# Optimization experiments

Measured on AMD Instinct MI355X. Metric: run time of the kernel, lower is better.

The kernel has to match this reference:

```python
import jax, jax.numpy as jnp
import numpy as np

B, S, H, NH, EHH, L = 8, 4, 50, 200, 400, 2
HID = 128
FDIM = 44 + 20 + 15          # 79: atom one-hot + amino-acid one-hot + position one-hot
EDIM = 2 * FDIM + 3          # h_i, h_j, distance, bond, t -> 161


def setup_inputs() -> dict:
    key = jax.random.key(0)
    ks = jax.random.split(key, 32)
    inp = {}
    inp["t"] = jax.random.uniform(ks[0], (B,), dtype=jnp.float32)
    inp["x_h"] = jax.random.normal(ks[1], (B, S, H, 3), dtype=jnp.float32)
    inp["x_heavy"] = jax.random.normal(ks[2], (B, 1, NH, 3), dtype=jnp.float32)
    inp["bond_matrix_h_heavy"] = (jax.random.uniform(ks[3], (B, H, NH)) < 0.02).astype(jnp.float32)
    inp["edge_mask_h_heavy"] = jnp.ones((B, H, NH), jnp.float32)
    inp["edge_mask_h_h"] = jnp.ones((B, EHH), jnp.float32)
    inp["atom_mask"] = jnp.ones((B, H, 1), jnp.float32)
    sc = 0.02
    shapes = {"W1": (L, EDIM, HID), "b1": (L, HID), "W2": (L, HID, HID), "b2": (L, HID),
              "Wc1": (L, HID, HID), "bc1": (L, HID), "Wc2": (L, HID, 1),
              "Wn1": (L, FDIM + HID, HID), "bn1": (L, HID), "Wn2": (L, HID, FDIM), "bn2": (L, FDIM)}
    for i, (n, s) in enumerate(shapes.items()):
        inp[n] = jax.random.normal(ks[4 + i], s, dtype=jnp.float32) * sc
    inp["peptide_seq"] = jax.random.randint(ks[20], (B, 15), 0, 20)
    inp["atom_labels_heavy"] = jax.random.randint(ks[21], (B, NH), 0, 44)
    inp["atom_labels_h"] = jax.random.randint(ks[22], (B, H), 0, 44)
    inp["amino_acid_pos_heavy"] = jax.random.randint(ks[23], (B, NH), 1, 16)
    inp["amino_acid_pos_h"] = jax.random.randint(ks[24], (B, H), 1, 16)
    inp["edges_h_h"] = jax.random.randint(ks[25], (B, EHH, 2), 0, H)
    inp["bound_atom"] = jax.random.randint(ks[26], (B, H), 0, NH)
    return inp


def _embed(labels, pos, peptide_seq):
    # one_hot(atom,44) ++ one_hot(seq[pos-1],20) ++ one_hot(pos-1,15)
    aa = jnp.take_along_axis(peptide_seq, pos - 1, axis=1)
    return jnp.concatenate([jax.nn.one_hot(labels, 44, dtype=jnp.float32),
                            jax.nn.one_hot(aa, 20, dtype=jnp.float32),
                            jax.nn.one_hot(pos - 1, 15, dtype=jnp.float32)], axis=-1)


def _gather_nodes(feat, idx):
    # feat [B,S,N,D], idx [B,E] -> [B,S,E,D]
    return jnp.take_along_axis(feat, idx[:, None, :, None], axis=2)


def _seg(data, ids, n):
    # data [B,S,E,D], ids [B,E] -> scatter-add over edges -> [B,S,n,D]
    f = jax.vmap(lambda d, i: jax.ops.segment_sum(jnp.swapaxes(d, 0, 1), i, num_segments=n))
    return jnp.swapaxes(f(data, ids), 1, 2)


def _forward(t, x_h, x_heavy, bond_hm, em_hheavy, em_hh, atom_mask,
             W1, b1, W2, b2, Wc1, bc1, Wc2, Wn1, bn1, Wn2, bn2,
             peptide_seq, atom_labels_heavy, atom_labels_h, pos_heavy, pos_h,
             edges_h_h, bound_atom):
    Bq, Sq, Hq, _ = x_h.shape
    Nh = x_heavy.shape[2]
    xhv = jnp.broadcast_to(x_heavy, (Bq, Sq, Nh, 3))
    emb_h = _embed(atom_labels_h, pos_h, peptide_seq)          # [B,H,79]
    emb_hv = _embed(atom_labels_heavy, pos_heavy, peptide_seq)  # [B,NH,79]
    # absolute coords: x_h relative to its bound heavy atom
    x_h_abs = x_h + jnp.take_along_axis(xhv, bound_atom[:, None, :, None], axis=2)
    x = jnp.concatenate([x_h_abs, xhv], axis=2)                 # [B,S,N,3]
    feat = jnp.concatenate([emb_h, emb_hv], axis=1)             # [B,N,79]
    feat = jnp.broadcast_to(feat[:, None], (Bq, Sq) + feat.shape[1:])
    bond = jnp.concatenate([jnp.zeros((Bq, Hq, Hq), bond_hm.dtype), bond_hm], axis=-1)  # [B,H,N]
    # edge indices: sparse h-h edges, then full h x heavy grid (row-major, cols offset by H)
    grid_r = jnp.repeat(jnp.arange(Hq), Nh)
    grid_c = Hq + jnp.tile(jnp.arange(Nh), Hq)
    edge_row = jnp.concatenate([edges_h_h[..., 0], jnp.broadcast_to(grid_r, (Bq, Hq * Nh))], axis=-1)
    edge_col = jnp.concatenate([edges_h_h[..., 1], jnp.broadcast_to(grid_c, (Bq, Hq * Nh))], axis=-1)
    emask = jnp.concatenate([em_hh, em_hheavy.reshape(Bq, -1)], axis=-1)[:, None, :, None]  # [B,1,E,1]
    bond_e = jax.vmap(lambda bm, r, c: bm[r, c])(bond, edge_row, edge_col)[:, None, :, None]
    x0 = x
    for l in range(W1.shape[0]):
        xi = _gather_nodes(x, edge_row)
        xj = _gather_nodes(x, edge_col)
        diff = xi - xj                                          # [B,S,E,3]
        dist = jnp.linalg.norm(diff, axis=-1, keepdims=True)    # [B,S,E,1]
        hi = _gather_nodes(feat, edge_row)
        hj = _gather_nodes(feat, edge_col)
        t_e = jnp.broadcast_to(t[:, None, None, None], dist.shape)
        ef = jnp.concatenate([hi, hj, dist, jnp.broadcast_to(bond_e, dist.shape), t_e], axis=-1)
        m = jax.nn.silu(ef @ W1[l] + b1[l])
        m = jax.nn.silu(m @ W2[l] + b2[l]) * emask              # masked messages [B,S,E,HID]
        cw = jax.nn.silu(m @ Wc1[l] + bc1[l]) @ Wc2[l]          # [B,S,E,1]
        agg_x = _seg(diff * cw, edge_row, Hq)                   # [B,S,H,3]
        agg_m = _seg(m, edge_row, Hq)                           # [B,S,H,HID]
        h_h = feat[:, :, :Hq]
        h_out = h_h + jax.nn.silu(jnp.concatenate([h_h, agg_m], axis=-1) @ Wn1[l] + bn1[l]) @ Wn2[l] + bn2[l]
        x = jnp.concatenate([x[:, :, :Hq] + agg_x, x[:, :, Hq:]], axis=2)
        feat = jnp.concatenate([h_out, feat[:, :, Hq:]], axis=2)
    pred = (x[:, :, :Hq] - x0[:, :, :Hq]) * atom_mask[:, None, :, :]
    return pred


def reference(t, x_h, x_heavy, bond_matrix_h_heavy, edge_mask_h_heavy, edge_mask_h_h, atom_mask,
              W1, b1, W2, b2, Wc1, bc1, Wc2, Wn1, bn1, Wn2, bn2,
              peptide_seq, atom_labels_heavy, atom_labels_h, amino_acid_pos_heavy, amino_acid_pos_h,
              edges_h_h, bound_atom):
    return _forward(t, x_h, x_heavy, bond_matrix_h_heavy, edge_mask_h_heavy, edge_mask_h_h, atom_mask,
                    W1, b1, W2, b2, Wc1, bc1, Wc2, Wn1, bn1, Wn2, bn2,
                    peptide_seq, atom_labels_heavy, atom_labels_h, amino_acid_pos_heavy, amino_acid_pos_h,
                    edges_h_h, bound_atom)
```

## Files before the change

### kernel.cpp

```cpp
#include <hip/hip_runtime.h>
#include <math.h>

#define B_     8
#define S_     4
#define H_     50
#define NH_    200
#define EHH_   400
#define L_     2
#define HID_   128
#define FDIM_  79
#define EDIM_  161
#define NN_    250
#define NROW_  1600
#define BS_    32
#define FS_    80
#define MSTR_  136
#define NDIM_  207
#define HVB_   1600

#define OFF_FEATH  0
#define OFF_X0     128000
#define OFF_X1     160000
#define OFF_X0H    192000
#define OFF_HHCOL  198400
#define OFF_HHEM   201600
#define OFF_HHOFF  204800
#define OFF_HIW1   205312
#define OFF_HJW1   614912
#define OFF_WP     1434112

typedef __attribute__((ext_vector_type(8))) short short8;
typedef __attribute__((ext_vector_type(4))) float f32x4;

__device__ __forceinline__ float silu_(float v) {
    return v * __builtin_amdgcn_rcpf(1.0f + __expf(-v));
}
__device__ __forceinline__ unsigned short f2bf(float f) {
    unsigned int u = __float_as_uint(f);
    unsigned int r = (u + 0x7fffu + ((u >> 16) & 1u)) >> 16;
    return (unsigned short)r;
}

#define HV_BLKS_    1600
#define PACK_BLKS_  256
#define SORT_BLKS_  8
#define HROW_BLKS_  200
#define FEAT_BLKS_  125
#define XI_BLKS_    32
#define SETUP_BLKS_ (HV_BLKS_ + PACK_BLKS_ + SORT_BLKS_ + HROW_BLKS_ + FEAT_BLKS_ + XI_BLKS_)

__global__ __launch_bounds__(256) void k_setup(
    const float* __restrict__ x_h, const float* __restrict__ x_hv,
    const int* __restrict__ bound,
    const int* __restrict__ ehh, const float* __restrict__ em_hh,
    const float* __restrict__ W1, const float* __restrict__ b1,
    const float* __restrict__ t_in,
    const float* __restrict__ W2, const float* __restrict__ Wc1,
    const int* __restrict__ lab_h, const int* __restrict__ pos_h,
    const int* __restrict__ lab_hv, const int* __restrict__ pos_hv,
    const int* __restrict__ pep,
    float* __restrict__ feat_h,
    float* __restrict__ x0, float* __restrict__ x1, float* __restrict__ x0h,
    int* __restrict__ hhcol, float* __restrict__ hhem, int* __restrict__ hhoff,
    float* __restrict__ hiW1, float* __restrict__ hjW1,
    unsigned short* __restrict__ Wp)
{
    int blk = blockIdx.x, t = threadIdx.x;
    if (blk < HV_BLKS_) {
        int g = blk*256 + t;
        int l = g / 204800;
        int r = g - l*204800;
        int node = r >> 7, col = r & 127;
        int b = node / NH_;
        int label = lab_hv[node], pos = pos_hv[node];
        int aa = pep[b*15 + pos - 1];
        const float* W1l = W1 + l*EDIM_*HID_;
        float hj = W1l[(FDIM_ + label)*HID_ + col]
                 + W1l[(FDIM_ + 44 + aa)*HID_ + col]
                 + W1l[(FDIM_ + 64 + pos - 1)*HID_ + col];
        hjW1[(size_t)(HVB_ + l*1600 + node)*HID_ + col] = hj;
        return;
    }
    blk -= HV_BLKS_;
    if (blk < PACK_BLKS_) {
        int g = blk*256 + t;
        int idx = g & 16383;
        int lm  = g >> 14;
        int l = lm >> 1, mat = lm & 1;
        int j   = idx & 7;
        int l15 = (idx >> 3) & 15;
        int qq  = (idx >> 7) & 3;
        int nt  = (idx >> 9) & 7;
        int kc  = (idx >> 12) & 3;
        int n = nt*16 + l15;
        int k = kc*32 + qq*8 + j;
        const float* W = (mat == 0 ? W2 : Wc1) + l*HID_*HID_;
        Wp[g] = f2bf(W[k*HID_ + n]);
        return;
    }
    blk -= PACK_BLKS_;
    if (blk < SORT_BLKS_) {
        int b = blk;
        __shared__ int scnt[64];
        __shared__ int srow[EHH_], scol[EHH_];
        __shared__ float sem[EHH_];
        if (t < 64) scnt[t] = 0;
        __syncthreads();
        for (int e = t; e < EHH_; e += 256) {
            int r = ehh[(b*EHH_ + e)*2 + 0];
            srow[e] = r;
            scol[e] = ehh[(b*EHH_ + e)*2 + 1];
            sem[e]  = em_hh[b*EHH_ + e];
            atomicAdd(&scnt[r], 1);
        }
        __syncthreads();
        if (t == 0) {
            int acc = 0;
            for (int i = 0; i < H_; ++i) { int v = scnt[i]; scnt[i] = acc; acc += v; }
        }
        __syncthreads();
        if (t < 51) hhoff[b*64 + t] = (t < H_) ? scnt[t] : EHH_;
        __syncthreads();
        for (int e = t; e < EHH_; e += 256) {
            int r = srow[e];
            int pos = atomicAdd(&scnt[r], 1);
            hhcol[b*EHH_ + pos] = scol[e];
            hhem [b*EHH_ + pos] = sem[e];
        }
        return;
    }
    blk -= SORT_BLKS_;
    if (blk < HROW_BLKS_) {
        int g = blk*256 + t;
        int node = g >> 7, col = g & 127;
        int b = node / H_;
        int label = lab_h[node], pos = pos_h[node];
        int aa = pep[b*15 + pos - 1];
        const float* W1l = W1;
        float hi = W1l[label*HID_ + col]
                 + W1l[(44 + aa)*HID_ + col]
                 + W1l[(64 + pos - 1)*HID_ + col]
                 + b1[col]
                 + t_in[b] * W1l[160*HID_ + col];
        float hj = W1l[(FDIM_ + label)*HID_ + col]
                 + W1l[(FDIM_ + 44 + aa)*HID_ + col]
                 + W1l[(FDIM_ + 64 + pos - 1)*HID_ + col];
        int h = node % H_;
        #pragma unroll
        for (int s = 0; s < S_; ++s) {
            int row = (b*S_ + s)*H_ + h;
            hiW1[(size_t)row*HID_ + col] = hi;
            hjW1[(size_t)row*HID_ + col] = hj;
        }
        return;
    }
    blk -= HROW_BLKS_;
    if (blk < FEAT_BLKS_) {
        int g = blk*256 + t;
        int node = g / FS_, f = g % FS_;
        int b = node / H_, h = node % H_;
        int label = lab_h[node], pos = pos_h[node];
        int aa = pep[b*15 + pos - 1];
        float v = 0.f;
        if (f < 44)      v = (f == label)          ? 1.0f : 0.0f;
        else if (f < 64) v = ((f - 44) == aa)      ? 1.0f : 0.0f;
        else if (f < 79) v = ((f - 64) == pos - 1) ? 1.0f : 0.0f;
        #pragma unroll
        for (int s = 0; s < S_; ++s)
            feat_h[((b*S_ + s)*H_ + h)*FS_ + f] = v;
        return;
    }
    blk -= FEAT_BLKS_;
    {
        int g = blk*256 + t;
        if (g >= BS_*NN_) return;
        int bs = g / NN_, n = g % NN_;
        int b = bs / S_;
        if (n < H_) {
            int ba = bound[b*H_ + n];
            for (int d = 0; d < 3; ++d) {
                float v = x_h[(bs*H_ + n)*3 + d] + x_hv[(b*NH_ + ba)*3 + d];
                x0[g*4 + d] = v;
                x0h[(bs*H_ + n)*4 + d] = v;
            }
        } else {
            int nh = n - H_;
            for (int d = 0; d < 3; ++d) {
                float v = x_hv[(b*NH_ + nh)*3 + d];
                x0[g*4 + d] = v;
                x1[g*4 + d] = v;
            }
        }
    }
}

__global__ __launch_bounds__(512) void k_edge_mlp(
    const float* __restrict__ xin, const float* __restrict__ hiW1g,
    const float* __restrict__ hjW1,
    const int* __restrict__ hhcol, const float* __restrict__ hhem,
    const int* __restrict__ hhoff,
    const float* __restrict__ em_hv, const float* __restrict__ bond_in,
    const float* __restrict__ W1,
    const float* __restrict__ b2, const float* __restrict__ bc1,
    const float* __restrict__ Wc2,
    const unsigned short* __restrict__ Wp, int l,
    const float* __restrict__ Wn1, const float* __restrict__ bn1,
    const float* __restrict__ Wn2, const float* __restrict__ bn2,
    const float* __restrict__ b1, const float* __restrict__ t_in,
    float* __restrict__ feat_h, float* __restrict__ xout,
    float* __restrict__ hiW1w, float* __restrict__ hjW1w,
    const float* __restrict__ x0h, const float* __restrict__ amask,
    float* __restrict__ out, int do_w1)
{
    __shared__ unsigned short s_wp[2*16384];
    __shared__ unsigned short s_m[8][16][MSTR_];
    __shared__ float s_hi[8][HID_];
    __shared__ float s_cc[5][HID_];
    __shared__ float s_mr[8][HID_];
    __shared__ float s_xr[8][4];

    const int t = threadIdx.x, lane = t & 63, w = t >> 6;
    const int l15 = lane & 15, q = lane >> 4;
    const int node0 = blockIdx.x*8;
    const int node  = node0 + w;
    const int bs = node / H_, h = node - bs*H_;
    const int b  = bs / S_;
    const int hb = (l ? 4800 : 0) + bs*H_;

    {
        const float4* src = (const float4*)(Wp + (size_t)l*32768);
        float4* dst = (float4*)s_wp;
        #pragma unroll
        for (int i = 0; i < 8; ++i) dst[t + i*512] = src[t + i*512];
    }
    const float* W1l = W1 + l*EDIM_*HID_;
    #pragma unroll
    for (int i = 0; i < 2; ++i) {
        int idx = i*512 + t;
        int g = idx >> 7, c = idx & 127;
        s_hi[g][c] = hiW1g[(size_t)(l*1600 + node0 + g)*HID_ + c];
    }
    if (t < 128) {
        s_cc[0][t] = W1l[158*HID_ + t];
        s_cc[1][t] = W1l[159*HID_ + t];
        s_cc[2][t] = b2 [l*HID_ + t];
        s_cc[3][t] = bc1[l*HID_ + t];
        s_cc[4][t] = Wc2[l*HID_ + t];
    }

    const int hh0 = hhoff[b*64 + h];
    const int cnt = hhoff[b*64 + h + 1] - hh0;
    const int E   = cnt + NH_;
    const int NT  = (E + 15) >> 4;

    const float xi0 = xin[(bs*NN_ + h)*4 + 0];
    const float xi1 = xin[(bs*NN_ + h)*4 + 1];
    const float xi2 = xin[(bs*NN_ + h)*4 + 2];

    auto gather = [&](int e, float& d0, float& d1, float& d2,
                      float& dist, float& bnd, float& em, int& jj) {
        if (e < E) {
            int col;
            if (e < cnt) {
                col = hhcol[b*EHH_ + hh0 + e];
                em  = hhem [b*EHH_ + hh0 + e];
                jj  = hb + col;
            } else {
                int cc = e - cnt;
                col = H_ + cc;
                em  = em_hv [(b*H_ + h)*NH_ + cc];
                bnd = bond_in[(b*H_ + h)*NH_ + cc];
                jj  = HVB_ + l*1600 + b*NH_ + cc;
            }
            d0 = xi0 - xin[(bs*NN_ + col)*4 + 0];
            d1 = xi1 - xin[(bs*NN_ + col)*4 + 1];
            d2 = xi2 - xin[(bs*NN_ + col)*4 + 2];
            dist = sqrtf(d0*d0 + d1*d1 + d2*d2);
        }
    };

    float macc[8] = {0.f,0.f,0.f,0.f,0.f,0.f,0.f,0.f};
    float xacc = 0.f;
    __syncthreads();

    float cd0=0.f, cd1=0.f, cd2=0.f, cdist=0.f, cbnd=0.f, cem=0.f;
    int   cjj = hb;
    if (lane < 16) gather(lane, cd0, cd1, cd2, cdist, cbnd, cem, cjj);
    float distb = __shfl(cdist, l15, 64);
    float bndb  = __shfl(cbnd,  l15, 64);
    int   jjb   = __shfl(cjj,   l15, 64);
    float4 pr[8];
    {
        const float* pj = hjW1 + (size_t)jjb*HID_ + q*8;
        #pragma unroll
        for (int kc = 0; kc < 4; ++kc) {
            pr[2*kc]   = *(const float4*)(pj + kc*32);
            pr[2*kc+1] = *(const float4*)(pj + kc*32 + 4);
        }
    }

    for (int ti = 0; ti < NT; ++ti) {
        const int nx = ti + 1;
        const bool hasNext = (nx < NT);

        float nd0=0.f, nd1=0.f, nd2=0.f, ndist=0.f, nbnd=0.f, nem=0.f;
        int   njj = hb;
        if (hasNext && lane < 16)
            gather(nx*16 + lane, nd0, nd1, nd2, ndist, nbnd, nem, njj);

        short8 afrag[4];
        #pragma unroll
        for (int kc = 0; kc < 4; ++kc) {
            int k0 = kc*32 + q*8;
            float4 c0 = pr[2*kc];
            float4 c1 = pr[2*kc+1];
            float4 h0 = *(const float4*)&s_hi[w][k0];
            float4 h1 = *(const float4*)&s_hi[w][k0 + 4];
            float4 wa0= *(const float4*)&s_cc[0][k0];
            float4 wa1= *(const float4*)&s_cc[0][k0 + 4];
            float4 wb0= *(const float4*)&s_cc[1][k0];
            float4 wb1= *(const float4*)&s_cc[1][k0 + 4];
            short8 fr;
            fr[0] = (short)f2bf(silu_(h0.x + c0.x + distb*wa0.x + bndb*wb0.x));
            fr[1] = (short)f2bf(silu_(h0.y + c0.y + distb*wa0.y + bndb*wb0.y));
            fr[2] = (short)f2bf(silu_(h0.z + c0.z + distb*wa0.z + bndb*wb0.z));
            fr[3] = (short)f2bf(silu_(h0.w + c0.w + distb*wa0.w + bndb*wb0.w));
            fr[4] = (short)f2bf(silu_(h1.x + c1.x + distb*wa1.x + bndb*wb1.x));
            fr[5] = (short)f2bf(silu_(h1.y + c1.y + distb*wa1.y + bndb*wb1.y));
            fr[6] = (short)f2bf(silu_(h1.z + c1.z + distb*wa1.z + bndb*wb1.z));
            fr[7] = (short)f2bf(silu_(h1.w + c1.w + distb*wa1.w + bndb*wb1.w));
            afrag[kc] = fr;
        }

        float ndistb = 0.f, nbndb = 0.f;
        if (hasNext) {
            ndistb = __shfl(ndist, l15, 64);
            nbndb  = __shfl(nbnd,  l15, 64);
            int njjb = __shfl(njj, l15, 64);
            const float* pj = hjW1 + (size_t)njjb*HID_ + q*8;
            #pragma unroll
            for (int kc = 0; kc < 4; ++kc) {
                pr[2*kc]   = *(const float4*)(pj + kc*32);
                pr[2*kc+1] = *(const float4*)(pj + kc*32 + 4);
            }
        }

        float em4[4];
        #pragma unroll
        for (int rr = 0; rr < 4; ++rr) em4[rr] = __shfl(cem, q*4 + rr, 64);
        #pragma unroll
        for (int nt = 0; nt < 8; ++nt) {
            float bias = s_cc[2][nt*16 + l15];
            f32x4 c = {bias, bias, bias, bias};
            #pragma unroll
            for (int kc = 0; kc < 4; ++kc) {
                short8 bf = *(const short8*)&s_wp[((kc*8 + nt)*64 + lane)*8];
                c = __builtin_amdgcn_mfma_f32_16x16x32_bf16(afrag[kc], bf, c, 0, 0, 0);
            }
            #pragma unroll
            for (int rr = 0; rr < 4; ++rr) {
                float mv = silu_(c[rr]) * em4[rr];
                s_m[w][q*4 + rr][nt*16 + l15] = f2bf(mv);
                macc[nt] += mv;
            }
        }
        __builtin_amdgcn_wave_barrier();

        short8 af2[4];
        #pragma unroll
        for (int kc = 0; kc < 4; ++kc)
            af2[kc] = *(const short8*)&s_m[w][l15][kc*32 + q*8];
        float p[4] = {0.f, 0.f, 0.f, 0.f};
        #pragma unroll
        for (int nt = 0; nt < 8; ++nt) {
            float bias = s_cc[3][nt*16 + l15];
            f32x4 c = {bias, bias, bias, bias};
            #pragma unroll
            for (int kc = 0; kc < 4; ++kc) {
                short8 bf = *(const short8*)&s_wp[16384 + ((kc*8 + nt)*64 + lane)*8];
                c = __builtin_amdgcn_mfma_f32_16x16x32_bf16(af2[kc], bf, c, 0, 0, 0);
            }
            float wcv = s_cc[4][nt*16 + l15];
            #pragma unroll
            for (int rr = 0; rr < 4; ++rr)
                p[rr] += silu_(c[rr]) * wcv;
        }
        #pragma unroll
        for (int m = 1; m < 16; m <<= 1) {
            #pragma unroll
            for (int rr = 0; rr < 4; ++rr) p[rr] += __shfl_xor(p[rr], m, 64);
        }
        #pragma unroll
        for (int rr = 0; rr < 4; ++rr) {
            float sd0 = __shfl(cd0, q*4 + rr, 64);
            float sd1 = __shfl(cd1, q*4 + rr, 64);
            float sd2 = __shfl(cd2, q*4 + rr, 64);
            if (l15 < 3) {
                float dsel = (l15 == 0) ? sd0 : ((l15 == 1) ? sd1 : sd2);
                xacc += dsel * p[rr];
            }
        }
        __builtin_amdgcn_wave_barrier();

        cd0 = nd0; cd1 = nd1; cd2 = nd2; cem = nem;
        distb = ndistb; bndb = nbndb;
    }

    #pragma unroll
    for (int nt = 0; nt < 8; ++nt) {
        macc[nt] += __shfl_xor(macc[nt], 16, 64);
        macc[nt] += __shfl_xor(macc[nt], 32, 64);
    }
    if (q == 0) {
        #pragma unroll
        for (int nt = 0; nt < 8; ++nt) s_mr[w][nt*16 + l15] = macc[nt];
    }
    xacc += __shfl_xor(xacc, 16, 64);
    xacc += __shfl_xor(xacc, 32, 64);
    if (q == 0 && l15 < 3) s_xr[w][l15] = xacc;
    __syncthreads();

    float* su = (float*)s_wp;
    for (int idx = t; idx < 8*208; idx += 512) {
        int g = idx / 208, k = idx - g*208;
        float v;
        if (k < FDIM_) v = feat_h[(node0 + g)*FS_ + k];
        else           v = s_mr[g][k - FDIM_];
        su[g*208 + k] = v;
    }
    __syncthreads();
    {
        const float* Wn1l = Wn1 + l*NDIM_*HID_;
        #pragma unroll
        for (int pass = 0; pass < 2; ++pass) {
            int task = pass*512 + t;
            int g = task >> 7, c = task & 127;
            const float* sp = su + g*208;
            const float* wp = Wn1l + c;
            float acc = 0.f;
            #pragma unroll 8
            for (int k = 0; k < NDIM_; ++k)
                acc += sp[k] * wp[(size_t)k*HID_];
            su[2048 + task] = silu_(acc + bn1[l*HID_ + c]);
        }
    }
    __syncthreads();
    {
        const float* Wn2l = Wn2 + l*HID_*FDIM_;
        #pragma unroll
        for (int pass = 0; pass < 2; ++pass) {
            int task = pass*512 + t;
            int g = task >> 7, c = task & 127;
            if (c < FDIM_) {
                const float* up = su + 2048 + g*HID_;
                const float* wp = Wn2l + c;
                float acc = bn2[l*FDIM_ + c];
                #pragma unroll 8
                for (int k = 0; k < HID_; ++k)
                    acc += up[k] * wp[(size_t)k*FDIM_];
                float nf = su[g*208 + c] + acc;
                feat_h[(node0 + g)*FS_ + c] = nf;
                su[g*208 + c] = nf;
            }
        }
    }
    if (t < 24) {
        int g = t / 3, d = t - (t/3)*3;
        int ng = node0 + g;
        int bsg = ng / H_, hg = ng - bsg*H_;
        float xv = xin[(bsg*NN_ + hg)*4 + d] + s_xr[g][d];
        if (do_w1) {
            xout[(bsg*NN_ + hg)*4 + d] = xv;
        } else {
            int bg = bsg / S_;
            out[ng*3 + d] = (xv - x0h[ng*4 + d]) * amask[bg*H_ + hg];
        }
    }
    if (!do_w1) return;
    __syncthreads();
    {
        const float* W1n = W1 + EDIM_*HID_;
        #pragma unroll
        for (int pass = 0; pass < 4; ++pass) {
            int task = pass*512 + t;
            int c = task & 127, g = (task >> 7) & 7, sel = task >> 10;
            const float* sp = su + g*208;
            const float* wp = W1n + (size_t)(sel ? FDIM_ : 0)*HID_ + c;
            float acc = 0.f;
            #pragma unroll 8
            for (int f = 0; f < FDIM_; ++f)
                acc += sp[f] * wp[(size_t)f*HID_];
            int ng = node0 + g;
            if (sel == 0) {
                int bg = (ng / H_) / S_;
                hiW1w[(size_t)(1600 + ng)*HID_ + c] =
                    acc + b1[HID_ + c] + t_in[bg]*W1n[160*HID_ + c];
            } else {
                hjW1w[(size_t)(4800 + ng)*HID_ + c] = acc;
            }
        }
    }
}

extern "C" void kernel_launch(void* const* d_in, const int* in_sizes, int n_in,
                              void* d_out, int out_size, void* d_ws, size_t ws_size,
                              hipStream_t stream)
{
    const float* t_in  = (const float*)d_in[0];
    const float* x_h   = (const float*)d_in[1];
    const float* x_hv  = (const float*)d_in[2];
    const float* bond  = (const float*)d_in[3];
    const float* em_hv = (const float*)d_in[4];
    const float* em_hh = (const float*)d_in[5];
    const float* amask = (const float*)d_in[6];
    const float* W1    = (const float*)d_in[7];
    const float* b1    = (const float*)d_in[8];
    const float* W2    = (const float*)d_in[9];
    const float* b2    = (const float*)d_in[10];
    const float* Wc1   = (const float*)d_in[11];
    const float* bc1   = (const float*)d_in[12];
    const float* Wc2   = (const float*)d_in[13];
    const float* Wn1   = (const float*)d_in[14];
    const float* bn1   = (const float*)d_in[15];
    const float* Wn2   = (const float*)d_in[16];
    const float* bn2   = (const float*)d_in[17];
    const int* pep     = (const int*)d_in[18];
    const int* lab_hv  = (const int*)d_in[19];
    const int* lab_h   = (const int*)d_in[20];
    const int* pos_hv  = (const int*)d_in[21];
    const int* pos_h   = (const int*)d_in[22];
    const int* ehh     = (const int*)d_in[23];
    const int* bound   = (const int*)d_in[24];

    float* ws     = (float*)d_ws;
    float* feat_h = ws + OFF_FEATH;
    float* x0     = ws + OFF_X0;
    float* x1     = ws + OFF_X1;
    float* x0h    = ws + OFF_X0H;
    int*   hhcol  = (int*)(ws + OFF_HHCOL);
    float* hhem   = ws + OFF_HHEM;
    int*   hhoff  = (int*)(ws + OFF_HHOFF);
    float* hiW1   = ws + OFF_HIW1;
    float* hjW1   = ws + OFF_HJW1;
    unsigned short* Wp = (unsigned short*)(ws + OFF_WP);

    hipLaunchKernelGGL(k_setup, dim3(SETUP_BLKS_), dim3(256), 0, stream,
                       x_h, x_hv, bound, ehh, em_hh,
                       W1, b1, t_in, W2, Wc1,
                       lab_h, pos_h, lab_hv, pos_hv, pep,
                       feat_h, x0, x1, x0h, hhcol, hhem, hhoff,
                       hiW1, hjW1, Wp);

    hipLaunchKernelGGL(k_edge_mlp, dim3(NROW_/8), dim3(512), 0, stream,
                       x0, hiW1, hjW1, hhcol, hhem, hhoff, em_hv, bond,
                       W1, b2, bc1, Wc2, Wp, 0,
                       Wn1, bn1, Wn2, bn2, b1, t_in,
                       feat_h, x1, hiW1, hjW1, x0h, amask,
                       (float*)d_out, 1);

    hipLaunchKernelGGL(k_edge_mlp, dim3(NROW_/8), dim3(512), 0, stream,
                       x1, hiW1, hjW1, hhcol, hhem, hhoff, em_hv, bond,
                       W1, b2, bc1, Wc2, Wp, 1,
                       Wn1, bn1, Wn2, bn2, b1, t_in,
                       feat_h, x1, hiW1, hjW1, x0h, amask,
                       (float*)d_out, 0);
}
```

Baseline: 322.7 us.

## Process two edge tiles per loop iteration to interleave independent MFMA chains

The per-node edge loop now handles two 16-edge tiles per iteration (A and B). It gathers and prefetches both tiles' data together and runs their two MFMA accumulator chains interleaved, so each B-fragment loaded from shared memory is reused by both. The intent is to hide MFMA dependency latency and halve the per-tile loop overhead and weight-fragment LDS reads. In exchange it doubles the s_m scratch in shared memory and raises register pressure. It also relies on an odd tile count being safe, with the extra tile gathering padded or masked edges.

```diff
diff --git a/kernel.cpp b/kernel.cpp
--- a/kernel.cpp
+++ b/kernel.cpp
@@ -213,7 +213,7 @@
     float* __restrict__ out, int do_w1)
 {
     __shared__ unsigned short s_wp[2*16384];
-    __shared__ unsigned short s_m[8][16][MSTR_];
+    __shared__ unsigned short s_m[8][2][16][MSTR_];
     __shared__ float s_hi[8][HID_];
     __shared__ float s_cc[5][HID_];
     __shared__ float s_mr[8][HID_];
@@ -283,127 +283,177 @@
     float xacc = 0.f;
     __syncthreads();
 
-    float cd0=0.f, cd1=0.f, cd2=0.f, cdist=0.f, cbnd=0.f, cem=0.f;
-    int   cjj = hb;
-    if (lane < 16) gather(lane, cd0, cd1, cd2, cdist, cbnd, cem, cjj);
-    float distb = __shfl(cdist, l15, 64);
-    float bndb  = __shfl(cbnd,  l15, 64);
-    int   jjb   = __shfl(cjj,   l15, 64);
-    float4 pr[8];
+    float cd0A=0.f, cd1A=0.f, cd2A=0.f, cdistA=0.f, cbndA=0.f, cemA=0.f;
+    float cd0B=0.f, cd1B=0.f, cd2B=0.f, cdistB=0.f, cbndB=0.f, cemB=0.f;
+    int   cjjA = hb, cjjB = hb;
+    if (lane < 16) {
+        gather(lane,      cd0A, cd1A, cd2A, cdistA, cbndA, cemA, cjjA);
+        gather(16 + lane, cd0B, cd1B, cd2B, cdistB, cbndB, cemB, cjjB);
+    }
+    float distbA = __shfl(cdistA, l15, 64), bndbA = __shfl(cbndA, l15, 64);
+    float distbB = __shfl(cdistB, l15, 64), bndbB = __shfl(cbndB, l15, 64);
+    int   jjbA   = __shfl(cjjA, l15, 64),   jjbB  = __shfl(cjjB, l15, 64);
+    float4 prA[8], prB[8];
     {
-        const float* pj = hjW1 + (size_t)jjb*HID_ + q*8;
+        const float* pjA = hjW1 + (size_t)jjbA*HID_ + q*8;
+        const float* pjB = hjW1 + (size_t)jjbB*HID_ + q*8;
         #pragma unroll
         for (int kc = 0; kc < 4; ++kc) {
-            pr[2*kc]   = *(const float4*)(pj + kc*32);
-            pr[2*kc+1] = *(const float4*)(pj + kc*32 + 4);
-        }
-    }
-
-    for (int ti = 0; ti < NT; ++ti) {
-        const int nx = ti + 1;
-        const bool hasNext = (nx < NT);
-
-        float nd0=0.f, nd1=0.f, nd2=0.f, ndist=0.f, nbnd=0.f, nem=0.f;
-        int   njj = hb;
-        if (hasNext && lane < 16)
-            gather(nx*16 + lane, nd0, nd1, nd2, ndist, nbnd, nem, njj);
-
-        short8 afrag[4];
+            prA[2*kc]   = *(const float4*)(pjA + kc*32);
+            prA[2*kc+1] = *(const float4*)(pjA + kc*32 + 4);
+            prB[2*kc]   = *(const float4*)(pjB + kc*32);
+            prB[2*kc+1] = *(const float4*)(pjB + kc*32 + 4);
+        }
+    }
+
+    for (int ti = 0; ti < NT; ti += 2) {
+        const bool hasNext = (ti + 2 < NT);
+
+        float ndA0=0.f, ndA1=0.f, ndA2=0.f, ndistA=0.f, nbndA=0.f, nemA=0.f;
+        float ndB0=0.f, ndB1=0.f, ndB2=0.f, ndistB=0.f, nbndB=0.f, nemB=0.f;
+        int   njjA = hb, njjB = hb;
+        if (hasNext && lane < 16) {
+            gather((ti + 2)*16 + lane, ndA0, ndA1, ndA2, ndistA, nbndA, nemA, njjA);
+            gather((ti + 3)*16 + lane, ndB0, ndB1, ndB2, ndistB, nbndB, nemB, njjB);
+        }
+
+        short8 afragA[4], afragB[4];
         #pragma unroll
         for (int kc = 0; kc < 4; ++kc) {
             int k0 = kc*32 + q*8;
-            float4 c0 = pr[2*kc];
-            float4 c1 = pr[2*kc+1];
             float4 h0 = *(const float4*)&s_hi[w][k0];
             float4 h1 = *(const float4*)&s_hi[w][k0 + 4];
             float4 wa0= *(const float4*)&s_cc[0][k0];
             float4 wa1= *(const float4*)&s_cc[0][k0 + 4];
             float4 wb0= *(const float4*)&s_cc[1][k0];
             float4 wb1= *(const float4*)&s_cc[1][k0 + 4];
-            short8 fr;
-            fr[0] = (short)f2bf(silu_(h0.x + c0.x + distb*wa0.x + bndb*wb0.x));
-            fr[1] = (short)f2bf(silu_(h0.y + c0.y + distb*wa0.y + bndb*wb0.y));
-            fr[2] = (short)f2bf(silu_(h0.z + c0.z + distb*wa0.z + bndb*wb0.z));
-            fr[3] = (short)f2bf(silu_(h0.w + c0.w + distb*wa0.w + bndb*wb0.w));
-            fr[4] = (short)f2bf(silu_(h1.x + c1.x + distb*wa1.x + bndb*wb1.x));
-            fr[5] = (short)f2bf(silu_(h1.y + c1.y + distb*wa1.y + bndb*wb1.y));
-            fr[6] = (short)f2bf(silu_(h1.z + c1.z + distb*wa1.z + bndb*wb1.z));
-            fr[7] = (short)f2bf(silu_(h1.w + c1.w + distb*wa1.w + bndb*wb1.w));
-            afrag[kc] = fr;
-        }
-
-        float ndistb = 0.f, nbndb = 0.f;
+            {
+                float4 c0 = prA[2*kc], c1 = prA[2*kc+1];
+                short8 fr;
+                fr[0] = (short)f2bf(silu_(h0.x + c0.x + distbA*wa0.x + bndbA*wb0.x));
+                fr[1] = (short)f2bf(silu_(h0.y + c0.y + distbA*wa0.y + bndbA*wb0.y));
+                fr[2] = (short)f2bf(silu_(h0.z + c0.z + distbA*wa0.z + bndbA*wb0.z));
+                fr[3] = (short)f2bf(silu_(h0.w + c0.w + distbA*wa0.w + bndbA*wb0.w));
+                fr[4] = (short)f2bf(silu_(h1.x + c1.x + distbA*wa1.x + bndbA*wb1.x));
+                fr[5] = (short)f2bf(silu_(h1.y + c1.y + distbA*wa1.y + bndbA*wb1.y));
+                fr[6] = (short)f2bf(silu_(h1.z + c1.z + distbA*wa1.z + bndbA*wb1.z));
+                fr[7] = (short)f2bf(silu_(h1.w + c1.w + distbA*wa1.w + bndbA*wb1.w));
+                afragA[kc] = fr;
+            }
+            {
+                float4 c0 = prB[2*kc], c1 = prB[2*kc+1];
+                short8 fr;
+                fr[0] = (short)f2bf(silu_(h0.x + c0.x + distbB*wa0.x + bndbB*wb0.x));
+                fr[1] = (short)f2bf(silu_(h0.y + c0.y + distbB*wa0.y + bndbB*wb0.y));
+                fr[2] = (short)f2bf(silu_(h0.z + c0.z + distbB*wa0.z + bndbB*wb0.z));
+                fr[3] = (short)f2bf(silu_(h0.w + c0.w + distbB*wa0.w + bndbB*wb0.w));
+                fr[4] = (short)f2bf(silu_(h1.x + c1.x + distbB*wa1.x + bndbB*wb1.x));
+                fr[5] = (short)f2bf(silu_(h1.y + c1.y + distbB*wa1.y + bndbB*wb1.y));
+                fr[6] = (short)f2bf(silu_(h1.z + c1.z + distbB*wa1.z + bndbB*wb1.z));
+                fr[7] = (short)f2bf(silu_(h1.w + c1.w + distbB*wa1.w + bndbB*wb1.w));
+                afragB[kc] = fr;
+            }
+        }
+
+        float ndistbA = 0.f, nbndbA = 0.f, ndistbB = 0.f, nbndbB = 0.f;
         if (hasNext) {
-            ndistb = __shfl(ndist, l15, 64);
-            nbndb  = __shfl(nbnd,  l15, 64);
-            int njjb = __shfl(njj, l15, 64);
-            const float* pj = hjW1 + (size_t)njjb*HID_ + q*8;
+            ndistbA = __shfl(ndistA, l15, 64); nbndbA = __shfl(nbndA, l15, 64);
+            ndistbB = __shfl(ndistB, l15, 64); nbndbB = __shfl(nbndB, l15, 64);
+            int njjbA = __shfl(njjA, l15, 64);
+            int njjbB = __shfl(njjB, l15, 64);
+            const float* pjA = hjW1 + (size_t)njjbA*HID_ + q*8;
+            const float* pjB = hjW1 + (size_t)njjbB*HID_ + q*8;
             #pragma unroll
             for (int kc = 0; kc < 4; ++kc) {
-                pr[2*kc]   = *(const float4*)(pj + kc*32);
-                pr[2*kc+1] = *(const float4*)(pj + kc*32 + 4);
-            }
-        }
-
-        float em4[4];
-        #pragma unroll
-        for (int rr = 0; rr < 4; ++rr) em4[rr] = __shfl(cem, q*4 + rr, 64);
+                prA[2*kc]   = *(const float4*)(pjA + kc*32);
+                prA[2*kc+1] = *(const float4*)(pjA + kc*32 + 4);
+                prB[2*kc]   = *(const float4*)(pjB + kc*32);
+                prB[2*kc+1] = *(const float4*)(pjB + kc*32 + 4);
+            }
+        }
+
+        float em4A[4], em4B[4];
+        #pragma unroll
+        for (int rr = 0; rr < 4; ++rr) {
+            em4A[rr] = __shfl(cemA, q*4 + rr, 64);
+            em4B[rr] = __shfl(cemB, q*4 + rr, 64);
+        }
         #pragma unroll
         for (int nt = 0; nt < 8; ++nt) {
             float bias = s_cc[2][nt*16 + l15];
-            f32x4 c = {bias, bias, bias, bias};
+            f32x4 cA = {bias, bias, bias, bias};
+            f32x4 cB = {bias, bias, bias, bias};
             #pragma unroll
             for (int kc = 0; kc < 4; ++kc) {
                 short8 bf = *(const short8*)&s_wp[((kc*8 + nt)*64 + lane)*8];
-                c = __builtin_amdgcn_mfma_f32_16x16x32_bf16(afrag[kc], bf, c, 0, 0, 0);
+                cA = __builtin_amdgcn_mfma_f32_16x16x32_bf16(afragA[kc], bf, cA, 0, 0, 0);
+                cB = __builtin_amdgcn_mfma_f32_16x16x32_bf16(afragB[kc], bf, cB, 0, 0, 0);
             }
             #pragma unroll
             for (int rr = 0; rr < 4; ++rr) {
-                float mv = silu_(c[rr]) * em4[rr];
-                s_m[w][q*4 + rr][nt*16 + l15] = f2bf(mv);
-                macc[nt] += mv;
+                float mvA = silu_(cA[rr]) * em4A[rr];
+                float mvB = silu_(cB[rr]) * em4B[rr];
+                s_m[w][0][q*4 + rr][nt*16 + l15] = f2bf(mvA);
+                s_m[w][1][q*4 + rr][nt*16 + l15] = f2bf(mvB);
+                macc[nt] += mvA + mvB;
             }
         }
         __builtin_amdgcn_wave_barrier();
 
-        short8 af2[4];
-        #pragma unroll
-        for (int kc = 0; kc < 4; ++kc)
-            af2[kc] = *(const short8*)&s_m[w][l15][kc*32 + q*8];
-        float p[4] = {0.f, 0.f, 0.f, 0.f};
+        short8 af2A[4], af2B[4];
+        #pragma unroll
+        for (int kc = 0; kc < 4; ++kc) {
+            af2A[kc] = *(const short8*)&s_m[w][0][l15][kc*32 + q*8];
+            af2B[kc] = *(const short8*)&s_m[w][1][l15][kc*32 + q*8];
+        }
+        float pA[4] = {0.f, 0.f, 0.f, 0.f};
+        float pB[4] = {0.f, 0.f, 0.f, 0.f};
         #pragma unroll
         for (int nt = 0; nt < 8; ++nt) {
             float bias = s_cc[3][nt*16 + l15];
-            f32x4 c = {bias, bias, bias, bias};
+            f32x4 cA = {bias, bias, bias, bias};
+            f32x4 cB = {bias, bias, bias, bias};
             #pragma unroll
             for (int kc = 0; kc < 4; ++kc) {
                 short8 bf = *(const short8*)&s_wp[16384 + ((kc*8 + nt)*64 + lane)*8];
-                c = __builtin_amdgcn_mfma_f32_16x16x32_bf16(af2[kc], bf, c, 0, 0, 0);
+                cA = __builtin_amdgcn_mfma_f32_16x16x32_bf16(af2A[kc], bf, cA, 0, 0, 0);
+                cB = __builtin_amdgcn_mfma_f32_16x16x32_bf16(af2B[kc], bf, cB, 0, 0, 0);
             }
             float wcv = s_cc[4][nt*16 + l15];
             #pragma unroll
-            for (int rr = 0; rr < 4; ++rr)
-                p[rr] += silu_(c[rr]) * wcv;
+            for (int rr = 0; rr < 4; ++rr) {
+                pA[rr] += silu_(cA[rr]) * wcv;
+                pB[rr] += silu_(cB[rr]) * wcv;
+            }
         }
         #pragma unroll
         for (int m = 1; m < 16; m <<= 1) {
             #pragma unroll
-            for (int rr = 0; rr < 4; ++rr) p[rr] += __shfl_xor(p[rr], m, 64);
+            for (int rr = 0; rr < 4; ++rr) {
+                pA[rr] += __shfl_xor(pA[rr], m, 64);
+                pB[rr] += __shfl_xor(pB[rr], m, 64);
+            }
         }
         #pragma unroll
         for (int rr = 0; rr < 4; ++rr) {
-            float sd0 = __shfl(cd0, q*4 + rr, 64);
-            float sd1 = __shfl(cd1, q*4 + rr, 64);
-            float sd2 = __shfl(cd2, q*4 + rr, 64);
+            float sd0A = __shfl(cd0A, q*4 + rr, 64);
+            float sd1A = __shfl(cd1A, q*4 + rr, 64);
+            float sd2A = __shfl(cd2A, q*4 + rr, 64);
+            float sd0B = __shfl(cd0B, q*4 + rr, 64);
+            float sd1B = __shfl(cd1B, q*4 + rr, 64);
+            float sd2B = __shfl(cd2B, q*4 + rr, 64);
             if (l15 < 3) {
-                float dsel = (l15 == 0) ? sd0 : ((l15 == 1) ? sd1 : sd2);
-                xacc += dsel * p[rr];
+                float dA = (l15 == 0) ? sd0A : ((l15 == 1) ? sd1A : sd2A);
+                float dB = (l15 == 0) ? sd0B : ((l15 == 1) ? sd1B : sd2B);
+                xacc += dA * pA[rr] + dB * pB[rr];
             }
         }
         __builtin_amdgcn_wave_barrier();
 
-        cd0 = nd0; cd1 = nd1; cd2 = nd2; cem = nem;
-        distb = ndistb; bndb = nbndb;
+        cd0A = ndA0; cd1A = ndA1; cd2A = ndA2; cemA = nemA;
+        cd0B = ndB0; cd1B = ndB1; cd2B = ndB2; cemB = nemB;
+        distbA = ndistbA; bndbA = nbndbA;
+        distbB = ndistbB; bndbB = nbndbB;
     }
 
     #pragma unroll
```

Result: slower. 406.3 us (+25.9%).

## Split each node's edge tiles across two waves and stream second weight from global

Applied to the files above, without the earlier changes.

Each block now handles 4 nodes instead of 8, and two waves share one node by taking alternate 16-edge tiles, with partial message and coordinate sums combined in shared memory. The grid doubles to 400 blocks to fill more CUs on a small problem. The second MFMA weight matrix is no longer staged in LDS and is read from global/L2 instead, halving that LDS buffer to raise occupancy. The cost is more global weight traffic per tile and doubled per-block setup (weight staging, node MLP) across more blocks.

```diff
diff --git a/kernel.cpp b/kernel.cpp
--- a/kernel.cpp
+++ b/kernel.cpp
@@ -212,17 +212,19 @@
     const float* __restrict__ x0h, const float* __restrict__ amask,
     float* __restrict__ out, int do_w1)
 {
-    __shared__ unsigned short s_wp[2*16384];
+    __shared__ unsigned short s_wp[16384];
     __shared__ unsigned short s_m[8][16][MSTR_];
-    __shared__ float s_hi[8][HID_];
+    __shared__ float s_hi[4][HID_];
     __shared__ float s_cc[5][HID_];
     __shared__ float s_mr[8][HID_];
     __shared__ float s_xr[8][4];
 
     const int t = threadIdx.x, lane = t & 63, w = t >> 6;
     const int l15 = lane & 15, q = lane >> 4;
-    const int node0 = blockIdx.x*8;
-    const int node  = node0 + w;
+    const int node0 = blockIdx.x*4;
+    const int rw    = w >> 1;
+    const int half  = w & 1;
+    const int node  = node0 + rw;
     const int bs = node / H_, h = node - bs*H_;
     const int b  = bs / S_;
     const int hb = (l ? 4800 : 0) + bs*H_;
@@ -231,13 +233,12 @@
         const float4* src = (const float4*)(Wp + (size_t)l*32768);
         float4* dst = (float4*)s_wp;
         #pragma unroll
-        for (int i = 0; i < 8; ++i) dst[t + i*512] = src[t + i*512];
-    }
+        for (int i = 0; i < 8; ++i) dst[i*512 + t] = src[i*512 + t];
+    }
+    const unsigned short* Wp3g = Wp + (size_t)l*32768 + 16384;
     const float* W1l = W1 + l*EDIM_*HID_;
-    #pragma unroll
-    for (int i = 0; i < 2; ++i) {
-        int idx = i*512 + t;
-        int g = idx >> 7, c = idx & 127;
+    if (t < 512) {
+        int g = t >> 7, c = t & 127;
         s_hi[g][c] = hiW1g[(size_t)(l*1600 + node0 + g)*HID_ + c];
     }
     if (t < 128) {
@@ -285,7 +286,7 @@
 
     float cd0=0.f, cd1=0.f, cd2=0.f, cdist=0.f, cbnd=0.f, cem=0.f;
     int   cjj = hb;
-    if (lane < 16) gather(lane, cd0, cd1, cd2, cdist, cbnd, cem, cjj);
+    if (lane < 16) gather(half*16 + lane, cd0, cd1, cd2, cdist, cbnd, cem, cjj);
     float distb = __shfl(cdist, l15, 64);
     float bndb  = __shfl(cbnd,  l15, 64);
     int   jjb   = __shfl(cjj,   l15, 64);
@@ -299,8 +300,8 @@
         }
     }
 
-    for (int ti = 0; ti < NT; ++ti) {
-        const int nx = ti + 1;
+    for (int ti = half; ti < NT; ti += 2) {
+        const int nx = ti + 2;
         const bool hasNext = (nx < NT);
 
         float nd0=0.f, nd1=0.f, nd2=0.f, ndist=0.f, nbnd=0.f, nem=0.f;
@@ -314,8 +315,8 @@
             int k0 = kc*32 + q*8;
             float4 c0 = pr[2*kc];
             float4 c1 = pr[2*kc+1];
-            float4 h0 = *(const float4*)&s_hi[w][k0];
-            float4 h1 = *(const float4*)&s_hi[w][k0 + 4];
+            float4 h0 = *(const float4*)&s_hi[rw][k0];
+            float4 h1 = *(const float4*)&s_hi[rw][k0 + 4];
             float4 wa0= *(const float4*)&s_cc[0][k0];
             float4 wa1= *(const float4*)&s_cc[0][k0 + 4];
             float4 wb0= *(const float4*)&s_cc[1][k0];
@@ -377,7 +378,7 @@
             f32x4 c = {bias, bias, bias, bias};
             #pragma unroll
             for (int kc = 0; kc < 4; ++kc) {
-                short8 bf = *(const short8*)&s_wp[16384 + ((kc*8 + nt)*64 + lane)*8];
+                short8 bf = *(const short8*)&Wp3g[((kc*8 + nt)*64 + lane)*8];
                 c = __builtin_amdgcn_mfma_f32_16x16x32_bf16(af2[kc], bf, c, 0, 0, 0);
             }
             float wcv = s_cc[4][nt*16 + l15];
@@ -421,54 +422,51 @@
     __syncthreads();
 
     float* su = (float*)s_wp;
-    for (int idx = t; idx < 8*208; idx += 512) {
+    for (int idx = t; idx < 4*208; idx += 512) {
         int g = idx / 208, k = idx - g*208;
         float v;
         if (k < FDIM_) v = feat_h[(node0 + g)*FS_ + k];
-        else           v = s_mr[g][k - FDIM_];
+        else {
+            int c = k - FDIM_;
+            v = s_mr[2*g][c] + s_mr[2*g + 1][c];
+        }
         su[g*208 + k] = v;
     }
     __syncthreads();
     {
         const float* Wn1l = Wn1 + l*NDIM_*HID_;
-        #pragma unroll
-        for (int pass = 0; pass < 2; ++pass) {
-            int task = pass*512 + t;
-            int g = task >> 7, c = task & 127;
-            const float* sp = su + g*208;
-            const float* wp = Wn1l + c;
-            float acc = 0.f;
-            #pragma unroll 8
-            for (int k = 0; k < NDIM_; ++k)
-                acc += sp[k] * wp[(size_t)k*HID_];
-            su[2048 + task] = silu_(acc + bn1[l*HID_ + c]);
-        }
+        int g = t >> 7, c = t & 127;
+        const float* sp = su + g*208;
+        const float* wp = Wn1l + c;
+        float acc = 0.f;
+        #pragma unroll 8
+        for (int k = 0; k < NDIM_; ++k)
+            acc += sp[k] * wp[(size_t)k*HID_];
+        su[1024 + t] = silu_(acc + bn1[l*HID_ + c]);
     }
     __syncthreads();
     {
         const float* Wn2l = Wn2 + l*HID_*FDIM_;
-        #pragma unroll
-        for (int pass = 0; pass < 2; ++pass) {
-            int task = pass*512 + t;
-            int g = task >> 7, c = task & 127;
-            if (c < FDIM_) {
-                const float* up = su + 2048 + g*HID_;
-                const float* wp = Wn2l + c;
-                float acc = bn2[l*FDIM_ + c];
-                #pragma unroll 8
-                for (int k = 0; k < HID_; ++k)
-                    acc += up[k] * wp[(size_t)k*FDIM_];
-                float nf = su[g*208 + c] + acc;
-                feat_h[(node0 + g)*FS_ + c] = nf;
-                su[g*208 + c] = nf;
-            }
-        }
-    }
-    if (t < 24) {
-        int g = t / 3, d = t - (t/3)*3;
+        int g = t >> 7, c = t & 127;
+        if (c < FDIM_) {
+            const float* up = su + 1024 + g*HID_;
+            const float* wp = Wn2l + c;
+            float acc = bn2[l*FDIM_ + c];
+            #pragma unroll 8
+            for (int k = 0; k < HID_; ++k)
+                acc += up[k] * wp[(size_t)k*FDIM_];
+            float nf = su[g*208 + c] + acc;
+            feat_h[(node0 + g)*FS_ + c] = nf;
+            su[g*208 + c] = nf;
+        }
+    }
+    if (t >= 128 && t < 140) {
+        int ix = t - 128;
+        int g = ix / 3, d = ix - (ix/3)*3;
         int ng = node0 + g;
         int bsg = ng / H_, hg = ng - bsg*H_;
-        float xv = xin[(bsg*NN_ + hg)*4 + d] + s_xr[g][d];
+        float xv = xin[(bsg*NN_ + hg)*4 + d]
+                 + s_xr[2*g][d] + s_xr[2*g + 1][d];
         if (do_w1) {
             xout[(bsg*NN_ + hg)*4 + d] = xv;
         } else {
@@ -481,9 +479,9 @@
     {
         const float* W1n = W1 + EDIM_*HID_;
         #pragma unroll
-        for (int pass = 0; pass < 4; ++pass) {
+        for (int pass = 0; pass < 2; ++pass) {
             int task = pass*512 + t;
-            int c = task & 127, g = (task >> 7) & 7, sel = task >> 10;
+            int c = task & 127, g = (task >> 7) & 3, sel = task >> 9;
             const float* sp = su + g*208;
             const float* wp = W1n + (size_t)(sel ? FDIM_ : 0)*HID_ + c;
             float acc = 0.f;
@@ -551,14 +549,14 @@
                        feat_h, x0, x1, x0h, hhcol, hhem, hhoff,
                        hiW1, hjW1, Wp);
 
-    hipLaunchKernelGGL(k_edge_mlp, dim3(NROW_/8), dim3(512), 0, stream,
+    hipLaunchKernelGGL(k_edge_mlp, dim3(NROW_/4), dim3(512), 0, stream,
                        x0, hiW1, hjW1, hhcol, hhem, hhoff, em_hv, bond,
                        W1, b2, bc1, Wc2, Wp, 0,
                        Wn1, bn1, Wn2, bn2, b1, t_in,
                        feat_h, x1, hiW1, hjW1, x0h, amask,
                        (float*)d_out, 1);
 
-    hipLaunchKernelGGL(k_edge_mlp, dim3(NROW_/8), dim3(512), 0, stream,
+    hipLaunchKernelGGL(k_edge_mlp, dim3(NROW_/4), dim3(512), 0, stream,
                        x1, hiW1, hjW1, hhcol, hhem, hhoff, em_hv, bond,
                        W1, b2, bc1, Wc2, Wp, 1,
                        Wn1, bn1, Wn2, bn2, b1, t_in,
```

Result: slower. 512.5 us (+58.8%).
